# Kernel optimization log

Hardware: AMD Instinct MI355X
Metric: run time of the kernel (lower is better)

Reference implementation:

```python
import jax, jax.numpy as jnp
import numpy as np

B, L, E = 2, 8192, 1024
H, D = 16, 64          # num_heads, head_dim (E = H*D)
C = 256                # chunk_size
EPS = 1e-6
LN_EPS = 1e-5


def setup_inputs() -> dict:
    key = jax.random.key(0)
    ks = jax.random.split(key, 12)
    w = lambda k, shape: (jax.random.normal(k, shape, jnp.float32) * 0.02)
    return {
        "x": jax.random.normal(ks[0], (B, L, E), jnp.float32),
        "Wq": w(ks[1], (E, E)), "bq": jnp.zeros((E,), jnp.float32),
        "Wk": w(ks[2], (E, E)), "bk": jnp.zeros((E,), jnp.float32),
        "Wv": w(ks[3], (E, E)), "bv": jnp.zeros((E,), jnp.float32),
        "Wo": w(ks[4], (E, E)), "bo": jnp.zeros((E,), jnp.float32),
        "gamma": jnp.ones((E,), jnp.float32),
        "beta": jnp.zeros((E,), jnp.float32),
    }


def _split_heads(t):
    # [B, L, E] -> [B, H, L, D]
    return t.reshape(B, L, H, D).transpose(0, 2, 1, 3)


def _phi(x):
    # feature map: elu(x) + 1  (strictly positive)
    return jax.nn.elu(x) + 1.0


def _chunkwise_linear_attention(q, k, v):
    """Causal linear attention via chunkwise parallel scan.

    q, k, v: [B, H, L, D] (q, k already feature-mapped, positive).
    out[t] = q_t @ S_t / (q_t . z_t), S_t = sum_{s<=t} k_s v_s^T, z_t = sum_{s<=t} k_s.
    """
    N = L // C
    # [N, B, H, C, D]
    qc = q.reshape(B, H, N, C, D).transpose(2, 0, 1, 3, 4)
    kc = k.reshape(B, H, N, C, D).transpose(2, 0, 1, 3, 4)
    vc = v.reshape(B, H, N, C, D).transpose(2, 0, 1, 3, 4)
    mask = jnp.tril(jnp.ones((C, C), q.dtype))  # causal within chunk (inclusive)

    def step(carry, inp):
        S, z = carry                      # S: [B,H,D,D], z: [B,H,D]
        qi, ki, vi = inp                  # [B,H,C,D]
        scores = jnp.einsum("bhcd,bhed->bhce", qi, ki) * mask  # [B,H,C,C]
        num = jnp.einsum("bhcd,bhde->bhce", qi, S) \
            + jnp.einsum("bhce,bhed->bhcd", scores, vi)
        den = jnp.einsum("bhcd,bhd->bhc", qi, z) + scores.sum(-1)
        out = num / (den + EPS)[..., None]
        S = S + jnp.einsum("bhcd,bhce->bhde", ki, vi)
        z = z + ki.sum(axis=2)
        return (S, z), out

    S0 = jnp.zeros((B, H, D, D), q.dtype)
    z0 = jnp.zeros((B, H, D), q.dtype)
    _, outs = jax.lax.scan(step, (S0, z0), (qc, kc, vc))
    # [N,B,H,C,D] -> [B,H,L,D]
    return outs.transpose(1, 2, 0, 3, 4).reshape(B, H, L, D)


def _layer_norm(x, gamma, beta):
    mu = x.mean(-1, keepdims=True)
    var = ((x - mu) ** 2).mean(-1, keepdims=True)
    return gamma * (x - mu) * jax.lax.rsqrt(var + LN_EPS) + beta


def reference(x, Wq, bq, Wk, bk, Wv, bv, Wo, bo, gamma, beta):
    residual = x
    q = _phi(_split_heads(x @ Wq + bq))
    k = _phi(_split_heads(x @ Wk + bk))
    v = _split_heads(x @ Wv + bv)
    out = _chunkwise_linear_attention(q, k, v)      # [B,H,L,D]
    out = out.transpose(0, 2, 1, 3).reshape(B, L, E)
    out = out @ Wo + bo
    return _layer_norm(out + residual, gamma, beta)
```

## Files before the change

kernel.cpp:

```cpp
#include <hip/hip_runtime.h>
#include <stdint.h>

typedef __attribute__((ext_vector_type(8))) short bf16x8;
typedef __attribute__((ext_vector_type(4))) float f32x4;
typedef __attribute__((ext_vector_type(2))) unsigned int u32x2;
typedef unsigned short u16;
typedef unsigned int u32;

#define MFMA16(a, b, c) __builtin_amdgcn_mfma_f32_16x16x32_bf16((a), (b), (c), 0, 0, 0)

__device__ __forceinline__ u16 f2bf(float f) {
  union { float f; u32 u; } c; c.f = f;
  u32 u = c.u;
  return (u16)((u + 0x7FFFu + ((u >> 16) & 1u)) >> 16);
}

__device__ __forceinline__ void gll16(const void* g, void* l) {
  __builtin_amdgcn_global_load_lds((__attribute__((address_space(1))) void*)(g),
                                   (__attribute__((address_space(3))) void*)(l),
                                   16, 0, 0);
}

__global__ __launch_bounds__(256) void cast_k(const float* __restrict__ x, u16* __restrict__ xb) {
  int idx = blockIdx.x * 256 + threadIdx.x;
#pragma unroll
  for (int it = 0; it < 4; it++) {
    size_t i = (size_t)idx + (size_t)it * 1048576;
    float4 v = ((const float4*)x)[i];
    u32x2 p;
    p.x = (u32)f2bf(v.x) | ((u32)f2bf(v.y) << 16);
    p.y = (u32)f2bf(v.z) | ((u32)f2bf(v.w) << 16);
    ((u32x2*)xb)[i] = p;
  }
}

__global__ __launch_bounds__(256) void wT_k(const float* __restrict__ Wq, const float* __restrict__ Wk,
                                            const float* __restrict__ Wv, const float* __restrict__ Wo,
                                            u16* __restrict__ wqkvT, u16* __restrict__ woT) {
  __shared__ float t[32][33];
  int which = blockIdx.z;
  const float* W = (which == 0) ? Wq : (which == 1) ? Wk : (which == 2) ? Wv : Wo;
  int k0 = blockIdx.y * 32, n0 = blockIdx.x * 32;
  int c = threadIdx.x & 31, r8 = threadIdx.x >> 5;
#pragma unroll
  for (int rr = 0; rr < 32; rr += 8)
    t[r8 + rr][c] = W[(size_t)(k0 + r8 + rr) * 1024 + n0 + c];
  __syncthreads();
  u16* outp = (which < 3) ? (wqkvT + (size_t)which * 1048576) : woT;
#pragma unroll
  for (int rr = 0; rr < 32; rr += 8)
    outp[(size_t)(n0 + r8 + rr) * 1024 + k0 + c] = f2bf(t[c][r8 + rr]);
}

template <int MODE>
__global__ __launch_bounds__(256, 2) void gemm_k(
    const u16* __restrict__ A, const u16* __restrict__ Bt,
    const float* __restrict__ b0, const float* __restrict__ b1, const float* __restrict__ b2,
    u16* __restrict__ q_o, u16* __restrict__ k_o, u16* __restrict__ kt_o, u16* __restrict__ vt_o,
    const float* __restrict__ xres, float* __restrict__ y_o) {
  __shared__ u16 As[128 * 32];
  __shared__ u16 Bs[128 * 32];
  const int tid = threadIdx.x;
  const int wave = tid >> 6, lane = tid & 63;
  const int quad = lane >> 4, l16 = lane & 15;
  const int wr = wave >> 1, wc = wave & 1;
  const int bn = blockIdx.x, bm = blockIdx.y;

  const int r_a = wave * 32 + (lane >> 2);
  const int c_a = (lane & 3) * 8;
  const size_t arow = (size_t)bm * 128;
  const size_t brow = (size_t)bn * 128;

  f32x4 zero = {0.f, 0.f, 0.f, 0.f};
  f32x4 acc[4][4];
#pragma unroll
  for (int i = 0; i < 4; i++)
#pragma unroll
    for (int j = 0; j < 4; j++) acc[i][j] = zero;

  for (int k0 = 0; k0 < 1024; k0 += 32) {
#pragma unroll
    for (int jc = 0; jc < 2; jc++) {
      int r = r_a + jc * 16;
      int lo = wave * 1024 + jc * 512 + lane * 8;
      gll16(A + (arow + r) * 1024 + k0 + c_a, &As[lo]);
      gll16(Bt + (brow + r) * 1024 + k0 + c_a, &Bs[lo]);
    }
    __syncthreads();
    bf16x8 af[4], bf[4];
#pragma unroll
    for (int t = 0; t < 4; t++) af[t] = *(const bf16x8*)&As[(wr * 64 + t * 16 + l16) * 32 + quad * 8];
#pragma unroll
    for (int t = 0; t < 4; t++) bf[t] = *(const bf16x8*)&Bs[(wc * 64 + t * 16 + l16) * 32 + quad * 8];
#pragma unroll
    for (int i = 0; i < 4; i++)
#pragma unroll
      for (int j = 0; j < 4; j++) acc[i][j] = MFMA16(af[i], bf[j], acc[i][j]);
    __syncthreads();
  }

  if (MODE == 0) {
#pragma unroll
    for (int i = 0; i < 4; i++) {
      const int m0 = bm * 128 + wr * 64 + i * 16 + quad * 4;
      const int b = m0 >> 13, l0 = m0 & 8191;
      const int nch = l0 >> 8, c0 = l0 & 255;
#pragma unroll
      for (int j = 0; j < 4; j++) {
        const int n_g = bn * 128 + wc * 64 + j * 16 + l16;
        const int sec = n_g >> 10, e = n_g & 1023;
        const float* bias = (sec == 0) ? b0 : ((sec == 1) ? b1 : b2);
        const float be = bias[e];
        float v4[4];
#pragma unroll
        for (int r = 0; r < 4; r++) {
          float v = acc[i][j][r] + be;
          if (sec < 2) v = (v > 0.f) ? (v + 1.f) : __expf(v);
          v4[r] = v;
        }
        const int h = e >> 6, d = e & 63;
        const int bh = b * 16 + h;
        if (sec <= 1) {
          u16* dst = (sec == 0) ? q_o : k_o;
          const size_t tb = (((size_t)bh * 8192 + l0) << 6) + d;
#pragma unroll
          for (int r = 0; r < 4; r++) dst[tb + (size_t)r * 64] = f2bf(v4[r]);
        }
        if (sec >= 1) {
          u16* dstT = (sec == 1) ? kt_o : vt_o;
          u32x2 p;
          p.x = (u32)f2bf(v4[0]) | ((u32)f2bf(v4[1]) << 16);
          p.y = (u32)f2bf(v4[2]) | ((u32)f2bf(v4[3]) << 16);
          *(u32x2*)&dstT[(((size_t)(bh * 32 + nch)) * 64 + d) * 256 + c0] = p;
        }
      }
    }
  } else {
#pragma unroll
    for (int i = 0; i < 4; i++) {
#pragma unroll
      for (int j = 0; j < 4; j++) {
#pragma unroll
        for (int r = 0; r < 4; r++) {
          int m_g = bm * 128 + wr * 64 + i * 16 + quad * 4 + r;
          int n_g = bn * 128 + wc * 64 + j * 16 + l16;
          float v = acc[i][j][r] + b0[n_g] + xres[(size_t)m_g * 1024 + n_g];
          y_o[(size_t)m_g * 1024 + n_g] = v;
        }
      }
    }
  }
}

__global__ __launch_bounds__(256) void phaseA_k(const u16* __restrict__ kt, const u16* __restrict__ vt,
                                                float* __restrict__ ST, float* __restrict__ zc) {
  const int tid = threadIdx.x;
  const int wave = tid >> 6, lane = tid & 63;
  const int quad = lane >> 4, l16 = lane & 15;
  const int wr = wave >> 1, wc = wave & 1;
  const int bhn = blockIdx.x;
  const u16* ktc = kt + (size_t)bhn * 16384;
  const u16* vtc = vt + (size_t)bhn * 16384;

  f32x4 zero = {0.f, 0.f, 0.f, 0.f};
  f32x4 t4[2][2];
  f32x4 za[2];
#pragma unroll
  for (int i = 0; i < 2; i++) {
    za[i] = zero;
#pragma unroll
    for (int j = 0; j < 2; j++) t4[i][j] = zero;
  }
  bf16x8 ones;
#pragma unroll
  for (int j = 0; j < 8; j++) ones[j] = (short)0x3F80;

#pragma unroll
  for (int ks = 0; ks < 8; ks++) {
    bf16x8 av[2], bk2[2];
#pragma unroll
    for (int t = 0; t < 2; t++) av[t] = *(const bf16x8*)&vtc[(wr * 32 + t * 16 + l16) * 256 + ks * 32 + quad * 8];
#pragma unroll
    for (int t = 0; t < 2; t++) bk2[t] = *(const bf16x8*)&ktc[(wc * 32 + t * 16 + l16) * 256 + ks * 32 + quad * 8];
#pragma unroll
    for (int i = 0; i < 2; i++)
#pragma unroll
      for (int j = 0; j < 2; j++) t4[i][j] = MFMA16(av[i], bk2[j], t4[i][j]);
    if (wr == 0) {
#pragma unroll
      for (int j = 0; j < 2; j++) za[j] = MFMA16(ones, bk2[j], za[j]);
    }
  }
  float* Sg = ST + (size_t)bhn * 4096;
#pragma unroll
  for (int i = 0; i < 2; i++)
#pragma unroll
    for (int j = 0; j < 2; j++)
#pragma unroll
      for (int r = 0; r < 4; r++)
        Sg[(wr * 32 + i * 16 + quad * 4 + r) * 64 + wc * 32 + j * 16 + l16] = t4[i][j][r];
  if (wr == 0 && quad == 0) {
#pragma unroll
    for (int j = 0; j < 2; j++) zc[(size_t)bhn * 64 + wc * 32 + j * 16 + l16] = za[j][0];
  }
}

__global__ __launch_bounds__(256) void phaseB_k(const float* __restrict__ ST, const float* __restrict__ zc,
                                                u16* __restrict__ STp, u16* __restrict__ zp) {
  const int blk = blockIdx.x, tid = threadIdx.x;
  if (blk < 512) {
    const int bh = blk >> 4;
    const int e = ((blk & 15) << 8) + tid;
    const size_t base = (size_t)bh * 32 * 4096 + e;
    float run = 0.f;
#pragma unroll
    for (int n = 0; n < 32; n++) {
      float v = ST[base + (size_t)n * 4096];
      STp[base + (size_t)n * 4096] = f2bf(run);
      run += v;
    }
  } else {
    const int idx = (blk - 512) * 256 + tid;
    const int bh = idx >> 6, d = idx & 63;
    const size_t zb = (size_t)bh * 2048 + d;
    float run = 0.f;
#pragma unroll
    for (int n = 0; n < 32; n++) {
      float v = zc[zb + n * 64];
      zp[zb + n * 64] = f2bf(run);
      run += v;
    }
  }
}

__global__ __launch_bounds__(256, 2) void phaseC_k(const u16* __restrict__ qb, const u16* __restrict__ kb,
                                                   const u16* __restrict__ vt, const u16* __restrict__ STp,
                                                   const u16* __restrict__ zp, u16* __restrict__ ao) {
  __shared__ u16 P[4][64 * 72];
  const int tid = threadIdx.x;
  const int wave = tid >> 6, lane = tid & 63;
  const int quad = lane >> 4, l16 = lane & 15;
  const int bhn = blockIdx.x;
  const int bh = bhn >> 5, n = bhn & 31;
  const int b = bh >> 4, h = bh & 15;
  const size_t cbase = (size_t)bhn * 16384;
  const u16* qc = qb + cbase;
  const u16* kc = kb + cbase;
  const u16* vtc = vt + cbase;
  const u16* STg = STp + (size_t)bhn * 4096;
  const u16* zg = zp + (size_t)bhn * 64;

  f32x4 zero = {0.f, 0.f, 0.f, 0.f};
  f32x4 num[4][4];
  f32x4 den[4];
#pragma unroll
  for (int i = 0; i < 4; i++) {
    den[i] = zero;
#pragma unroll
    for (int j = 0; j < 4; j++) num[i][j] = zero;
  }
  bf16x8 ones;
#pragma unroll
  for (int j = 0; j < 8; j++) ones[j] = (short)0x3F80;

  bf16x8 aq[4][2];
#pragma unroll
  for (int i = 0; i < 4; i++)
#pragma unroll
    for (int ks = 0; ks < 2; ks++)
      aq[i][ks] = *(const bf16x8*)&qc[(wave * 64 + i * 16 + l16) * 64 + ks * 32 + quad * 8];

#pragma unroll
  for (int ks = 0; ks < 2; ks++) {
    bf16x8 bz = *(const bf16x8*)&zg[ks * 32 + quad * 8];
    bf16x8 bs[4];
#pragma unroll
    for (int j = 0; j < 4; j++) bs[j] = *(const bf16x8*)&STg[(j * 16 + l16) * 64 + ks * 32 + quad * 8];
#pragma unroll
    for (int i = 0; i < 4; i++) {
      den[i] = MFMA16(aq[i][ks], bz, den[i]);
#pragma unroll
      for (int j = 0; j < 4; j++) num[i][j] = MFMA16(aq[i][ks], bs[j], num[i][j]);
    }
  }

  u16* Pw = &P[wave][0];

  for (int cc = 0; cc <= wave; cc++) {
    bf16x8 bkf[2][4];
#pragma unroll
    for (int ks = 0; ks < 2; ks++)
#pragma unroll
      for (int j = 0; j < 4; j++)
        bkf[ks][j] = *(const bf16x8*)&kc[(cc * 64 + j * 16 + l16) * 64 + ks * 32 + quad * 8];
#pragma unroll
    for (int i = 0; i < 4; i++) {
      f32x4 sc4[4];
#pragma unroll
      for (int j = 0; j < 4; j++) sc4[j] = zero;
#pragma unroll
      for (int ks = 0; ks < 2; ks++)
#pragma unroll
        for (int j = 0; j < 4; j++) sc4[j] = MFMA16(aq[i][ks], bkf[ks][j], sc4[j]);
#pragma unroll
      for (int j = 0; j < 4; j++) {
#pragma unroll
        for (int r = 0; r < 4; r++) {
          int row = wave * 64 + i * 16 + quad * 4 + r;
          int col = cc * 64 + j * 16 + l16;
          float v = (col <= row) ? sc4[j][r] : 0.f;
          Pw[(i * 16 + quad * 4 + r) * 72 + j * 16 + l16] = f2bf(v);
        }
      }
    }
    bf16x8 bvf[2][4];
#pragma unroll
    for (int ks2 = 0; ks2 < 2; ks2++)
#pragma unroll
      for (int j = 0; j < 4; j++)
        bvf[ks2][j] = *(const bf16x8*)&vtc[(j * 16 + l16) * 256 + cc * 64 + ks2 * 32 + quad * 8];
#pragma unroll
    for (int i = 0; i < 4; i++) {
#pragma unroll
      for (int ks2 = 0; ks2 < 2; ks2++) {
        bf16x8 ap = *(const bf16x8*)&Pw[(i * 16 + l16) * 72 + ks2 * 32 + quad * 8];
#pragma unroll
        for (int j = 0; j < 4; j++) num[i][j] = MFMA16(ap, bvf[ks2][j], num[i][j]);
        den[i] = MFMA16(ap, ones, den[i]);
      }
    }
  }

#pragma unroll
  for (int i = 0; i < 4; i++)
#pragma unroll
    for (int j = 0; j < 4; j++)
#pragma unroll
      for (int r = 0; r < 4; r++) {
        int row = wave * 64 + i * 16 + quad * 4 + r;
        int col = j * 16 + l16;
        float o = num[i][j][r] / (den[i][r] + 1e-6f);
        int l = n * 256 + row;
        ao[(((size_t)b * 8192 + l) * 16 + h) * 64 + col] = f2bf(o);
      }
}

__global__ __launch_bounds__(256) void ln_k(const float* __restrict__ y, const float* __restrict__ gamma,
                                            const float* __restrict__ beta, float* __restrict__ o) {
  int row = blockIdx.x, tid = threadIdx.x;
  const float4* yv = (const float4*)(y + (size_t)row * 1024);
  float4 v = yv[tid];
  float s = v.x + v.y + v.z + v.w;
  float s2 = v.x * v.x + v.y * v.y + v.z * v.z + v.w * v.w;
#pragma unroll
  for (int off = 32; off; off >>= 1) {
    s += __shfl_down(s, off, 64);
    s2 += __shfl_down(s2, off, 64);
  }
  __shared__ float red[8];
  int wave = tid >> 6, lane = tid & 63;
  if (lane == 0) { red[wave] = s; red[4 + wave] = s2; }
  __syncthreads();
  s = red[0] + red[1] + red[2] + red[3];
  s2 = red[4] + red[5] + red[6] + red[7];
  float mu = s * 0.0009765625f;
  float var = s2 * 0.0009765625f - mu * mu;
  float inv = rsqrtf(var + 1e-5f);
  float4 g = ((const float4*)gamma)[tid];
  float4 bb = ((const float4*)beta)[tid];
  float4 ov;
  ov.x = g.x * (v.x - mu) * inv + bb.x;
  ov.y = g.y * (v.y - mu) * inv + bb.y;
  ov.z = g.z * (v.z - mu) * inv + bb.z;
  ov.w = g.w * (v.w - mu) * inv + bb.w;
  ((float4*)(o + (size_t)row * 1024))[tid] = ov;
}

extern "C" void kernel_launch(void* const* d_in, const int* in_sizes, int n_in,
                              void* d_out, int out_size, void* d_ws, size_t ws_size,
                              hipStream_t stream) {
  const float* x = (const float*)d_in[0];
  const float* Wq = (const float*)d_in[1];
  const float* bq = (const float*)d_in[2];
  const float* Wk = (const float*)d_in[3];
  const float* bk = (const float*)d_in[4];
  const float* Wv = (const float*)d_in[5];
  const float* bv = (const float*)d_in[6];
  const float* Wo = (const float*)d_in[7];
  const float* bo = (const float*)d_in[8];
  const float* gamma = (const float*)d_in[9];
  const float* beta = (const float*)d_in[10];

  char* ws = (char*)d_ws;
  u16* xb = (u16*)(ws + 0);
  u16* qb = (u16*)(ws + 33554432);
  u16* kb = (u16*)(ws + 67108864);
  u16* kt = (u16*)(ws + 100663296);
  u16* vt = (u16*)(ws + 134217728);
  u16* wqkvT = (u16*)(ws + 167772160);
  u16* woT = (u16*)(ws + 174063616);
  float* SchT = (float*)(ws + 176160768);
  float* zch = (float*)(ws + 192937984);
  u16* STp = (u16*)(ws + 193200128);
  u16* zp = (u16*)(ws + 201588736);
  u16* attno = kt;
  float* ypre = (float*)(ws + 0);

  cast_k<<<4096, 256, 0, stream>>>(x, xb);
  wT_k<<<dim3(32, 32, 4), 256, 0, stream>>>(Wq, Wk, Wv, Wo, wqkvT, woT);
  gemm_k<0><<<dim3(24, 128), 256, 0, stream>>>(xb, wqkvT, bq, bk, bv, qb, kb, kt, vt, nullptr, nullptr);
  phaseA_k<<<1024, 256, 0, stream>>>(kt, vt, SchT, zch);
  phaseB_k<<<520, 256, 0, stream>>>(SchT, zch, STp, zp);
  phaseC_k<<<1024, 256, 0, stream>>>(qb, kb, vt, STp, zp, attno);
  gemm_k<1><<<dim3(8, 128), 256, 0, stream>>>(attno, woT, bo, nullptr, nullptr, nullptr, nullptr, nullptr, nullptr,
                                              x, ypre);
  ln_k<<<16384, 256, 0, stream>>>(ypre, gamma, beta, (float*)d_out);
}
```

Baseline: 438.9 us.

## Drop transposed K output, use bf16 residual and pre-LN buffer, deepen GEMM K-step

The QKV GEMM no longer writes a transposed copy of K. phaseA instead transposes K per chunk through shared memory, which removes one full write stream. The output-projection GEMM now reads the bf16-cast x as its residual and writes its pre-LayerNorm result in bf16, and LN reads bf16, roughly halving that traffic. The GEMMs also load two 32-wide K slices per barrier and swap the grid axes so consecutive blocks walk M. The bf16 residual and intermediate add rounding error before LayerNorm.

```diff
diff --git a/kernel.cpp b/kernel.cpp
--- a/kernel.cpp
+++ b/kernel.cpp
@@ -13,6 +13,12 @@
   union { float f; u32 u; } c; c.f = f;
   u32 u = c.u;
   return (u16)((u + 0x7FFFu + ((u >> 16) & 1u)) >> 16);
+}
+
+__device__ __forceinline__ float bf2f(u16 h) {
+  union { u32 u; float f; } c;
+  c.u = ((u32)h) << 16;
+  return c.f;
 }
 
 __device__ __forceinline__ void gll16(const void* g, void* l) {
@@ -56,15 +62,15 @@
 __global__ __launch_bounds__(256, 2) void gemm_k(
     const u16* __restrict__ A, const u16* __restrict__ Bt,
     const float* __restrict__ b0, const float* __restrict__ b1, const float* __restrict__ b2,
-    u16* __restrict__ q_o, u16* __restrict__ k_o, u16* __restrict__ kt_o, u16* __restrict__ vt_o,
-    const float* __restrict__ xres, float* __restrict__ y_o) {
-  __shared__ u16 As[128 * 32];
-  __shared__ u16 Bs[128 * 32];
+    u16* __restrict__ q_o, u16* __restrict__ k_o, u16* __restrict__ vt_o,
+    const u16* __restrict__ xres, u16* __restrict__ y_o) {
+  __shared__ u16 As[2][4096];
+  __shared__ u16 Bs[2][4096];
   const int tid = threadIdx.x;
   const int wave = tid >> 6, lane = tid & 63;
   const int quad = lane >> 4, l16 = lane & 15;
   const int wr = wave >> 1, wc = wave & 1;
-  const int bn = blockIdx.x, bm = blockIdx.y;
+  const int bm = blockIdx.x, bn = blockIdx.y;
 
   const int r_a = wave * 32 + (lane >> 2);
   const int c_a = (lane & 3) * 8;
@@ -78,24 +84,31 @@
 #pragma unroll
     for (int j = 0; j < 4; j++) acc[i][j] = zero;
 
-  for (int k0 = 0; k0 < 1024; k0 += 32) {
-#pragma unroll
-    for (int jc = 0; jc < 2; jc++) {
-      int r = r_a + jc * 16;
-      int lo = wave * 1024 + jc * 512 + lane * 8;
-      gll16(A + (arow + r) * 1024 + k0 + c_a, &As[lo]);
-      gll16(Bt + (brow + r) * 1024 + k0 + c_a, &Bs[lo]);
+  for (int k0 = 0; k0 < 1024; k0 += 64) {
+#pragma unroll
+    for (int h = 0; h < 2; h++) {
+      const int kk = k0 + h * 32;
+#pragma unroll
+      for (int jc = 0; jc < 2; jc++) {
+        int r = r_a + jc * 16;
+        int lo = wave * 1024 + jc * 512 + lane * 8;
+        gll16(A + (arow + r) * 1024 + kk + c_a, &As[h][lo]);
+        gll16(Bt + (brow + r) * 1024 + kk + c_a, &Bs[h][lo]);
+      }
     }
     __syncthreads();
-    bf16x8 af[4], bf[4];
-#pragma unroll
-    for (int t = 0; t < 4; t++) af[t] = *(const bf16x8*)&As[(wr * 64 + t * 16 + l16) * 32 + quad * 8];
-#pragma unroll
-    for (int t = 0; t < 4; t++) bf[t] = *(const bf16x8*)&Bs[(wc * 64 + t * 16 + l16) * 32 + quad * 8];
-#pragma unroll
-    for (int i = 0; i < 4; i++)
-#pragma unroll
-      for (int j = 0; j < 4; j++) acc[i][j] = MFMA16(af[i], bf[j], acc[i][j]);
+#pragma unroll
+    for (int h = 0; h < 2; h++) {
+      bf16x8 af[4], bf[4];
+#pragma unroll
+      for (int t = 0; t < 4; t++) af[t] = *(const bf16x8*)&As[h][(wr * 64 + t * 16 + l16) * 32 + quad * 8];
+#pragma unroll
+      for (int t = 0; t < 4; t++) bf[t] = *(const bf16x8*)&Bs[h][(wc * 64 + t * 16 + l16) * 32 + quad * 8];
+#pragma unroll
+      for (int i = 0; i < 4; i++)
+#pragma unroll
+        for (int j = 0; j < 4; j++) acc[i][j] = MFMA16(af[i], bf[j], acc[i][j]);
+    }
     __syncthreads();
   }
 
@@ -120,18 +133,16 @@
         }
         const int h = e >> 6, d = e & 63;
         const int bh = b * 16 + h;
-        if (sec <= 1) {
-          u16* dst = (sec == 0) ? q_o : k_o;
-          const size_t tb = (((size_t)bh * 8192 + l0) << 6) + d;
-#pragma unroll
-          for (int r = 0; r < 4; r++) dst[tb + (size_t)r * 64] = f2bf(v4[r]);
-        }
-        if (sec >= 1) {
-          u16* dstT = (sec == 1) ? kt_o : vt_o;
+        if (sec == 2) {
           u32x2 p;
           p.x = (u32)f2bf(v4[0]) | ((u32)f2bf(v4[1]) << 16);
           p.y = (u32)f2bf(v4[2]) | ((u32)f2bf(v4[3]) << 16);
-          *(u32x2*)&dstT[(((size_t)(bh * 32 + nch)) * 64 + d) * 256 + c0] = p;
+          *(u32x2*)&vt_o[(((size_t)(bh * 32 + nch)) * 64 + d) * 256 + c0] = p;
+        } else {
+          u16* dst = (sec == 0) ? q_o : k_o;
+          const size_t tb = (((size_t)bh * 8192 + l0) << 6) + d;
+#pragma unroll
+          for (int r = 0; r < 4; r++) dst[tb + (size_t)r * 64] = f2bf(v4[r]);
         }
       }
     }
@@ -144,23 +155,37 @@
         for (int r = 0; r < 4; r++) {
           int m_g = bm * 128 + wr * 64 + i * 16 + quad * 4 + r;
           int n_g = bn * 128 + wc * 64 + j * 16 + l16;
-          float v = acc[i][j][r] + b0[n_g] + xres[(size_t)m_g * 1024 + n_g];
-          y_o[(size_t)m_g * 1024 + n_g] = v;
+          float v = acc[i][j][r] + b0[n_g] + bf2f(xres[(size_t)m_g * 1024 + n_g]);
+          y_o[(size_t)m_g * 1024 + n_g] = f2bf(v);
         }
       }
     }
   }
 }
 
-__global__ __launch_bounds__(256) void phaseA_k(const u16* __restrict__ kt, const u16* __restrict__ vt,
-                                                float* __restrict__ ST, float* __restrict__ zc) {
+__global__ __launch_bounds__(256, 2) void phaseA_k(const u16* __restrict__ kb, const u16* __restrict__ vt,
+                                                   float* __restrict__ ST, float* __restrict__ zc) {
+  __shared__ u16 kT[64 * 264];
   const int tid = threadIdx.x;
   const int wave = tid >> 6, lane = tid & 63;
   const int quad = lane >> 4, l16 = lane & 15;
   const int wr = wave >> 1, wc = wave & 1;
   const int bhn = blockIdx.x;
-  const u16* ktc = kt + (size_t)bhn * 16384;
+  const u16* kc = kb + (size_t)bhn * 16384;
   const u16* vtc = vt + (size_t)bhn * 16384;
+
+#pragma unroll
+  for (int t = 0; t < 2; t++) {
+    const int dblk = wave + 4 * t;
+#pragma unroll
+    for (int itc = 0; itc < 4; itc++) {
+      const int c = itc * 64 + lane;
+      bf16x8 kv = *(const bf16x8*)&kc[c * 64 + dblk * 8];
+#pragma unroll
+      for (int j = 0; j < 8; j++) kT[(dblk * 8 + j) * 264 + c] = (u16)kv[j];
+    }
+  }
+  __syncthreads();
 
   f32x4 zero = {0.f, 0.f, 0.f, 0.f};
   f32x4 t4[2][2];
@@ -181,7 +206,7 @@
 #pragma unroll
     for (int t = 0; t < 2; t++) av[t] = *(const bf16x8*)&vtc[(wr * 32 + t * 16 + l16) * 256 + ks * 32 + quad * 8];
 #pragma unroll
-    for (int t = 0; t < 2; t++) bk2[t] = *(const bf16x8*)&ktc[(wc * 32 + t * 16 + l16) * 256 + ks * 32 + quad * 8];
+    for (int t = 0; t < 2; t++) bk2[t] = *(const bf16x8*)&kT[(wc * 32 + t * 16 + l16) * 264 + ks * 32 + quad * 8];
 #pragma unroll
     for (int i = 0; i < 2; i++)
 #pragma unroll
@@ -345,13 +370,14 @@
       }
 }
 
-__global__ __launch_bounds__(256) void ln_k(const float* __restrict__ y, const float* __restrict__ gamma,
+__global__ __launch_bounds__(256) void ln_k(const u16* __restrict__ y, const float* __restrict__ gamma,
                                             const float* __restrict__ beta, float* __restrict__ o) {
   int row = blockIdx.x, tid = threadIdx.x;
-  const float4* yv = (const float4*)(y + (size_t)row * 1024);
-  float4 v = yv[tid];
-  float s = v.x + v.y + v.z + v.w;
-  float s2 = v.x * v.x + v.y * v.y + v.z * v.z + v.w * v.w;
+  u32x2 pv = ((const u32x2*)(y + (size_t)row * 1024))[tid];
+  float vx = bf2f((u16)(pv.x & 0xFFFF)), vy = bf2f((u16)(pv.x >> 16));
+  float vz = bf2f((u16)(pv.y & 0xFFFF)), vw = bf2f((u16)(pv.y >> 16));
+  float s = vx + vy + vz + vw;
+  float s2 = vx * vx + vy * vy + vz * vz + vw * vw;
 #pragma unroll
   for (int off = 32; off; off >>= 1) {
     s += __shfl_down(s, off, 64);
@@ -369,10 +395,10 @@
   float4 g = ((const float4*)gamma)[tid];
   float4 bb = ((const float4*)beta)[tid];
   float4 ov;
-  ov.x = g.x * (v.x - mu) * inv + bb.x;
-  ov.y = g.y * (v.y - mu) * inv + bb.y;
-  ov.z = g.z * (v.z - mu) * inv + bb.z;
-  ov.w = g.w * (v.w - mu) * inv + bb.w;
+  ov.x = g.x * (vx - mu) * inv + bb.x;
+  ov.y = g.y * (vy - mu) * inv + bb.y;
+  ov.z = g.z * (vz - mu) * inv + bb.z;
+  ov.w = g.w * (vw - mu) * inv + bb.w;
   ((float4*)(o + (size_t)row * 1024))[tid] = ov;
 }
 
@@ -395,7 +421,7 @@
   u16* xb = (u16*)(ws + 0);
   u16* qb = (u16*)(ws + 33554432);
   u16* kb = (u16*)(ws + 67108864);
-  u16* kt = (u16*)(ws + 100663296);
+  u16* attno = (u16*)(ws + 100663296);
   u16* vt = (u16*)(ws + 134217728);
   u16* wqkvT = (u16*)(ws + 167772160);
   u16* woT = (u16*)(ws + 174063616);
@@ -403,16 +429,15 @@
   float* zch = (float*)(ws + 192937984);
   u16* STp = (u16*)(ws + 193200128);
   u16* zp = (u16*)(ws + 201588736);
-  u16* attno = kt;
-  float* ypre = (float*)(ws + 0);
+  u16* ypre = qb;
 
   cast_k<<<4096, 256, 0, stream>>>(x, xb);
   wT_k<<<dim3(32, 32, 4), 256, 0, stream>>>(Wq, Wk, Wv, Wo, wqkvT, woT);
-  gemm_k<0><<<dim3(24, 128), 256, 0, stream>>>(xb, wqkvT, bq, bk, bv, qb, kb, kt, vt, nullptr, nullptr);
-  phaseA_k<<<1024, 256, 0, stream>>>(kt, vt, SchT, zch);
+  gemm_k<0><<<dim3(128, 24), 256, 0, stream>>>(xb, wqkvT, bq, bk, bv, qb, kb, vt, nullptr, nullptr);
+  phaseA_k<<<1024, 256, 0, stream>>>(kb, vt, SchT, zch);
   phaseB_k<<<520, 256, 0, stream>>>(SchT, zch, STp, zp);
   phaseC_k<<<1024, 256, 0, stream>>>(qb, kb, vt, STp, zp, attno);
-  gemm_k<1><<<dim3(8, 128), 256, 0, stream>>>(attno, woT, bo, nullptr, nullptr, nullptr, nullptr, nullptr, nullptr,
-                                              x, ypre);
+  gemm_k<1><<<dim3(128, 8), 256, 0, stream>>>(attno, woT, bo, nullptr, nullptr, nullptr, nullptr, nullptr, xb,
+                                              ypre);
   ln_k<<<16384, 256, 0, stream>>>(ypre, gamma, beta, (float*)d_out);
 }
```

Result: faster. 389.4 us (-11.3%).
